# Performance work log

Hardware: AMD Instinct MI355X
Metric: run time of the kernel (lower is better)

## Reference

```python
import jax, jax.numpy as jnp
import numpy as np

EMB = 64
N_NODES = 50000
N_EDGES = 800000

def _mlp(h, W1, b1, W2, b2):
    h = jax.nn.relu(h @ W1 + b1)
    return jax.nn.relu(h @ W2 + b2)

def setup_inputs() -> dict:
    key = jax.random.key(0)
    ks = jax.random.split(key, 12)
    s = 1.0 / np.sqrt(3 * EMB)
    s2 = 1.0 / np.sqrt(EMB)
    x = jax.random.normal(ks[0], (N_NODES, 2 * EMB), dtype=jnp.float32)
    edge_index = jax.random.randint(ks[1], (2, N_EDGES), 0, N_NODES, dtype=jnp.int32)
    edge_attr = jax.random.normal(ks[2], (N_EDGES, EMB), dtype=jnp.float32)
    u = jax.random.normal(ks[3], (64, 64), dtype=jnp.float32)
    batch = jax.random.randint(ks[4], (N_NODES,), 0, 64, dtype=jnp.int32)
    W1a = jax.random.uniform(ks[5], (3 * EMB, EMB), jnp.float32, -s, s)
    b1a = jax.random.uniform(ks[6], (EMB,), jnp.float32, -s, s)
    W1b = jax.random.uniform(ks[7], (EMB, EMB), jnp.float32, -s2, s2)
    b1b = jax.random.uniform(ks[8], (EMB,), jnp.float32, -s2, s2)
    W2a = jax.random.uniform(ks[9], (3 * EMB, EMB), jnp.float32, -s, s)
    b2a = jax.random.uniform(ks[10], (EMB,), jnp.float32, -s, s)
    W2b = jax.random.uniform(ks[11], (EMB, EMB), jnp.float32, -s2, s2)
    b2b = jax.random.uniform(jax.random.fold_in(key, 99), (EMB,), jnp.float32, -s2, s2)
    return {"x": x, "edge_index": edge_index, "edge_attr": edge_attr, "u": u, "batch": batch,
            "W1a": W1a, "b1a": b1a, "W1b": W1b, "b1b": b1b,
            "W2a": W2a, "b2a": b2a, "W2b": W2b, "b2b": b2b}

def reference(x, edge_index, edge_attr, u, batch, W1a, b1a, W1b, b1b, W2a, b2a, W2b, b2b):
    senders, receivers = edge_index[0], edge_index[1]
    # gather sender node features [E, 2*EMB] and concat edge features -> [E, 3*EMB]
    msg = jnp.concatenate([x[senders], edge_attr], axis=1)
    msg = _mlp(msg, W1a, b1a, W1b, b1b)  # [E, EMB]
    agg = jax.ops.segment_sum(msg, receivers, num_segments=x.shape[0])  # [N, EMB]
    h = jnp.concatenate([x, agg], axis=1)  # [N, 3*EMB]
    return _mlp(h, W2a, b2a, W2b, b2b)  # [N, EMB]
```

## Files before the change

### kernel.cpp

```cpp
#include <hip/hip_runtime.h>
#include <hip/hip_bf16.h>

typedef __attribute__((ext_vector_type(8))) __bf16 bf16x8;
typedef __attribute__((ext_vector_type(4))) __bf16 bf16x4;
typedef __attribute__((ext_vector_type(2))) __bf16 bf16x2;
typedef __attribute__((ext_vector_type(4))) float f32x4;

#define MFMA(a, b, c) __builtin_amdgcn_mfma_f32_16x16x32_bf16((a), (b), (c), 0, 0, 0)

__device__ __forceinline__ bf16x8 pack8(f32x4 a, f32x4 b) {
    bf16x8 r;
    r[0] = (__bf16)a[0]; r[1] = (__bf16)a[1]; r[2] = (__bf16)a[2]; r[3] = (__bf16)a[3];
    r[4] = (__bf16)b[0]; r[5] = (__bf16)b[1]; r[6] = (__bf16)b[2]; r[7] = (__bf16)b[3];
    return r;
}

__device__ __forceinline__ bf16x8 cvt8(const float* __restrict__ p) {
    return pack8(*(const f32x4*)(p), *(const f32x4*)(p + 4));
}

__global__ __launch_bounds__(256) void zero_i32(int* __restrict__ p, int n) {
    for (int i = blockIdx.x * blockDim.x + threadIdx.x; i < n;
         i += gridDim.x * blockDim.x)
        p[i] = 0;
}

__global__ __launch_bounds__(256) void precompute_y(
    const float* __restrict__ x,
    const float* __restrict__ W1a, const float* __restrict__ b1a,
    const float* __restrict__ W2a, const float* __restrict__ b2a,
    float* __restrict__ y1, float* __restrict__ y2,
    int N, int ntiles)
{
    const int LDK = 136;
    __shared__ __align__(16) __bf16 w1t[64 * 136];
    __shared__ __align__(16) __bf16 w2t[64 * 136];
    for (int idx = threadIdx.x; idx < 64 * 128; idx += 256) {
        int k = idx >> 6, n = idx & 63;
        w1t[n * LDK + k] = (__bf16)W1a[k * 64 + n];
        w2t[n * LDK + k] = (__bf16)W2a[k * 64 + n];
    }
    __syncthreads();

    const int lane = threadIdx.x & 63, wave = threadIdx.x >> 6;
    const int l15 = lane & 15, l4 = lane >> 4;

    f32x4 bias1[4], bias2[4];
#pragma unroll
    for (int nt = 0; nt < 4; ++nt) {
        bias1[nt] = *(const f32x4*)(b1a + nt * 16 + l4 * 4);
        bias2[nt] = *(const f32x4*)(b2a + nt * 16 + l4 * 4);
    }

    for (int tile = blockIdx.x * 4 + wave; tile < ntiles; tile += gridDim.x * 4) {
        const int node = tile * 16 + l15;
        const int nrow = min(node, N - 1);
        f32x4 acc1[4], acc2[4];
#pragma unroll
        for (int nt = 0; nt < 4; ++nt) {
            acc1[nt] = (f32x4){0.f, 0.f, 0.f, 0.f};
            acc2[nt] = (f32x4){0.f, 0.f, 0.f, 0.f};
        }
#pragma unroll
        for (int j = 0; j < 4; ++j) {
            const int k0 = j * 32 + l4 * 8;
            bf16x8 b = cvt8(x + (size_t)nrow * 128 + k0);
#pragma unroll
            for (int nt = 0; nt < 4; ++nt) {
                bf16x8 a1 = *(const bf16x8*)(w1t + (nt * 16 + l15) * LDK + k0);
                acc1[nt] = MFMA(a1, b, acc1[nt]);
                bf16x8 a2 = *(const bf16x8*)(w2t + (nt * 16 + l15) * LDK + k0);
                acc2[nt] = MFMA(a2, b, acc2[nt]);
            }
        }
        if (node < N) {
#pragma unroll
            for (int nt = 0; nt < 4; ++nt) {
                f32x4 v1 = acc1[nt] + bias1[nt];
                f32x4 v2 = acc2[nt] + bias2[nt];
                *(f32x4*)(y1 + (size_t)node * 64 + nt * 16 + l4 * 4) = v1;
                *(f32x4*)(y2 + (size_t)node * 64 + nt * 16 + l4 * 4) = v2;
            }
        }
    }
}

__global__ __launch_bounds__(256) void hist_kernel(
    const int* __restrict__ recv, int* __restrict__ cnt, int E)
{
    for (int e = blockIdx.x * blockDim.x + threadIdx.x; e < E;
         e += gridDim.x * blockDim.x)
        atomicAdd(&cnt[recv[e]], 1);
}

__global__ __launch_bounds__(1024) void scan_offsets(
    const int* __restrict__ cnt, int* __restrict__ offs, int* __restrict__ cur, int N)
{
    __shared__ int wsum[16];
    __shared__ int stot;
    const int tid = threadIdx.x;
    const int lane = tid & 63, wave = tid >> 6;
    int carry = 0;
    const int CH = 4096;
    for (int base = 0; base < N; base += CH) {
        const int idx = base + tid * 4;
        int v0 = (idx + 0 < N) ? cnt[idx + 0] : 0;
        int v1 = (idx + 1 < N) ? cnt[idx + 1] : 0;
        int v2 = (idx + 2 < N) ? cnt[idx + 2] : 0;
        int v3 = (idx + 3 < N) ? cnt[idx + 3] : 0;
        const int t = v0 + v1 + v2 + v3;
        int s = t;
#pragma unroll
        for (int d = 1; d < 64; d <<= 1) {
            int u = __shfl_up(s, d);
            if (lane >= d) s += u;
        }
        if (lane == 63) wsum[wave] = s;
        __syncthreads();
        if (wave == 0) {
            int w = (lane < 16) ? wsum[lane] : 0;
            int ws = w;
#pragma unroll
            for (int d = 1; d < 16; d <<= 1) {
                int u = __shfl_up(ws, d);
                if (lane >= d) ws += u;
            }
            if (lane < 16) wsum[lane] = ws - w;
            if (lane == 15) stot = ws;
        }
        __syncthreads();
        const int excl = s - t + wsum[wave] + carry;
        if (idx + 0 < N) { offs[idx+0] = excl;                cur[idx+0] = excl; }
        if (idx + 1 < N) { offs[idx+1] = excl+v0;             cur[idx+1] = excl+v0; }
        if (idx + 2 < N) { offs[idx+2] = excl+v0+v1;          cur[idx+2] = excl+v0+v1; }
        if (idx + 3 < N) { offs[idx+3] = excl+v0+v1+v2;       cur[idx+3] = excl+v0+v1+v2; }
        carry += stot;
        __syncthreads();
    }
    if (tid == 0) offs[N] = carry;
}

template<int MODE>
__global__ __launch_bounds__(256) void edge_mlp(
    const float* __restrict__ eattr,
    const int* __restrict__ send, const int* __restrict__ recv,
    const float* __restrict__ W1a, const float* __restrict__ W1b,
    const float* __restrict__ b1b,
    const float* __restrict__ y1,
    int* __restrict__ cur, __bf16* __restrict__ msgC, float* agg,
    int E, int ntiles)
{
    const int LDK = 72;
    __shared__ __align__(16) __bf16 wat[64 * 72];
    __shared__ __align__(16) __bf16 wbt[64 * 72];
    __shared__ __align__(16) __bf16 hbuf[4][16 * 72];
    for (int idx = threadIdx.x; idx < 64 * 64; idx += 256) {
        int k = idx >> 6, n = idx & 63;
        wat[n * LDK + k] = (__bf16)W1a[(128 + k) * 64 + n];
        wbt[n * LDK + k] = (__bf16)W1b[k * 64 + n];
    }
    __syncthreads();

    const int lane = threadIdx.x & 63, wave = threadIdx.x >> 6;
    const int l15 = lane & 15, l4 = lane >> 4;
    __bf16* hb = hbuf[wave];

    f32x4 biasb[4];
#pragma unroll
    for (int nt = 0; nt < 4; ++nt) biasb[nt] = *(const f32x4*)(b1b + nt * 16 + l4 * 4);

    int tile = blockIdx.x * 4 + wave;
    const int stride = gridDim.x * 4;
    if (tile >= ntiles) return;

    int e  = tile * 16 + l15;
    int el = min(e, E - 1);
    int s  = send[el];
    int rv = recv[el];
    f32x4 ea[4], cin[4];
    {
        const float* ep = eattr + (size_t)el * 64 + l4 * 8;
        ea[0] = *(const f32x4*)(ep);      ea[1] = *(const f32x4*)(ep + 4);
        ea[2] = *(const f32x4*)(ep + 32); ea[3] = *(const f32x4*)(ep + 36);
#pragma unroll
        for (int nt = 0; nt < 4; ++nt)
            cin[nt] = *(const f32x4*)(y1 + (size_t)s * 64 + nt * 16 + l4 * 4);
    }

    while (true) {
        const int tnext = tile + stride;
        const bool have_next = tnext < ntiles;
        int e_n = e, el_n = el, s_n = s, rv_n = rv;
        if (have_next) {
            e_n  = tnext * 16 + l15;
            el_n = min(e_n, E - 1);
            s_n  = send[el_n];
            rv_n = recv[el_n];
        }
        int p = 0;
        if (MODE == 0 && l4 == 0 && e < E) p = atomicAdd(&cur[rv], 1);

        f32x4 acc[4] = {cin[0], cin[1], cin[2], cin[3]};
#pragma unroll
        for (int j = 0; j < 2; ++j) {
            bf16x8 b = pack8(ea[2 * j], ea[2 * j + 1]);
            const int k0 = j * 32 + l4 * 8;
#pragma unroll
            for (int nt = 0; nt < 4; ++nt) {
                bf16x8 a = *(const bf16x8*)(wat + (nt * 16 + l15) * LDK + k0);
                acc[nt] = MFMA(a, b, acc[nt]);
            }
        }
        f32x4 ea_n[4], cin_n[4];
        if (have_next) {
            const float* ep = eattr + (size_t)el_n * 64 + l4 * 8;
            ea_n[0] = *(const f32x4*)(ep);      ea_n[1] = *(const f32x4*)(ep + 4);
            ea_n[2] = *(const f32x4*)(ep + 32); ea_n[3] = *(const f32x4*)(ep + 36);
#pragma unroll
            for (int nt = 0; nt < 4; ++nt)
                cin_n[nt] = *(const f32x4*)(y1 + (size_t)s_n * 64 + nt * 16 + l4 * 4);
        }
#pragma unroll
        for (int nt = 0; nt < 4; ++nt) {
            bf16x4 hv;
#pragma unroll
            for (int r = 0; r < 4; ++r) hv[r] = (__bf16)fmaxf(acc[nt][r], 0.f);
            *(bf16x4*)(hb + l15 * LDK + nt * 16 + l4 * 4) = hv;
        }
        f32x4 acc2[4];
#pragma unroll
        for (int nt = 0; nt < 4; ++nt) acc2[nt] = biasb[nt];
#pragma unroll
        for (int j = 0; j < 2; ++j) {
            const int k0 = j * 32 + l4 * 8;
            bf16x8 b = *(const bf16x8*)(hb + l15 * LDK + k0);
#pragma unroll
            for (int nt = 0; nt < 4; ++nt) {
                bf16x8 a = *(const bf16x8*)(wbt + (nt * 16 + l15) * LDK + k0);
                acc2[nt] = MFMA(a, b, acc2[nt]);
            }
        }
        if (MODE == 0) {
            const int pb = __shfl(p, l15);
            if (e < E) {
                __bf16* row = msgC + (size_t)pb * 64;
#pragma unroll
                for (int nt = 0; nt < 4; ++nt) {
                    bf16x4 mv;
#pragma unroll
                    for (int r = 0; r < 4; ++r) mv[r] = (__bf16)fmaxf(acc2[nt][r], 0.f);
                    *(bf16x4*)(row + nt * 16 + l4 * 4) = mv;
                }
            }
        } else {
            if (e < E) {
                float* base = agg + (size_t)rv * 64 + l4 * 4;
#pragma unroll
                for (int nt = 0; nt < 4; ++nt)
#pragma unroll
                    for (int r = 0; r < 4; ++r)
                        unsafeAtomicAdd(base + nt * 16 + r, fmaxf(acc2[nt][r], 0.f));
            }
        }
        if (!have_next) break;
        tile = tnext; e = e_n; el = el_n; s = s_n; rv = rv_n;
#pragma unroll
        for (int i = 0; i < 4; ++i) { ea[i] = ea_n[i]; cin[i] = cin_n[i]; }
    }
}

__global__ __launch_bounds__(256) void csr_reduce(
    const unsigned* __restrict__ msg_u,
    const int* __restrict__ offs,
    __bf16* __restrict__ aggB, int N)
{
    const int wave = threadIdx.x >> 6, lane = threadIdx.x & 63;
    const int half = lane >> 5, c = lane & 31;
    for (int node = blockIdx.x * 4 + wave; node < N; node += gridDim.x * 4) {
        const int oL = offs[node], oR = offs[node + 1];
        float ax = 0.f, ay = 0.f;
        for (int p = oL + half; p < oR; p += 2) {
            const unsigned u = msg_u[(size_t)p * 32 + c];
            ax += __uint_as_float(u << 16);
            ay += __uint_as_float(u & 0xffff0000u);
        }
        ax += __shfl_xor(ax, 32);
        ay += __shfl_xor(ay, 32);
        if (half == 0) {
            bf16x2 v; v[0] = (__bf16)ax; v[1] = (__bf16)ay;
            *(bf16x2*)(aggB + (size_t)node * 64 + c * 2) = v;
        }
    }
}

template<int AGGF32>
__global__ __launch_bounds__(256) void node_pass(
    const void* __restrict__ aggp,
    const float* __restrict__ W2a, const float* __restrict__ W2b,
    const float* __restrict__ b2b,
    const float* __restrict__ y2, float* __restrict__ out,
    int N, int ntiles)
{
    const int LDK = 72;
    __shared__ __align__(16) __bf16 wat[64 * 72];
    __shared__ __align__(16) __bf16 wbt[64 * 72];
    __shared__ __align__(16) __bf16 hbuf[4][16 * 72];
    for (int idx = threadIdx.x; idx < 64 * 64; idx += 256) {
        int k = idx >> 6, n = idx & 63;
        wat[n * LDK + k] = (__bf16)W2a[(128 + k) * 64 + n];
        wbt[n * LDK + k] = (__bf16)W2b[k * 64 + n];
    }
    __syncthreads();

    const int lane = threadIdx.x & 63, wave = threadIdx.x >> 6;
    const int l15 = lane & 15, l4 = lane >> 4;
    __bf16* hb = hbuf[wave];

    f32x4 biasb[4];
#pragma unroll
    for (int nt = 0; nt < 4; ++nt) biasb[nt] = *(const f32x4*)(b2b + nt * 16 + l4 * 4);

    for (int tile = blockIdx.x * 4 + wave; tile < ntiles; tile += gridDim.x * 4) {
        const int node = tile * 16 + l15;
        const int nrow = min(node, N - 1);

        f32x4 acc[4];
#pragma unroll
        for (int nt = 0; nt < 4; ++nt)
            acc[nt] = *(const f32x4*)(y2 + (size_t)nrow * 64 + nt * 16 + l4 * 4);
#pragma unroll
        for (int j = 0; j < 2; ++j) {
            const int k0 = j * 32 + l4 * 8;
            bf16x8 b;
            if (AGGF32) b = cvt8((const float*)aggp + (size_t)nrow * 64 + k0);
            else        b = *(const bf16x8*)((const __bf16*)aggp + (size_t)nrow * 64 + k0);
#pragma unroll
            for (int nt = 0; nt < 4; ++nt) {
                bf16x8 a = *(const bf16x8*)(wat + (nt * 16 + l15) * LDK + k0);
                acc[nt] = MFMA(a, b, acc[nt]);
            }
        }
#pragma unroll
        for (int nt = 0; nt < 4; ++nt) {
            bf16x4 hv;
#pragma unroll
            for (int r = 0; r < 4; ++r) hv[r] = (__bf16)fmaxf(acc[nt][r], 0.f);
            *(bf16x4*)(hb + l15 * LDK + nt * 16 + l4 * 4) = hv;
        }

        f32x4 acc2[4];
#pragma unroll
        for (int nt = 0; nt < 4; ++nt) acc2[nt] = biasb[nt];
#pragma unroll
        for (int j = 0; j < 2; ++j) {
            const int k0 = j * 32 + l4 * 8;
            bf16x8 b = *(const bf16x8*)(hb + l15 * LDK + k0);
#pragma unroll
            for (int nt = 0; nt < 4; ++nt) {
                bf16x8 a = *(const bf16x8*)(wbt + (nt * 16 + l15) * LDK + k0);
                acc2[nt] = MFMA(a, b, acc2[nt]);
            }
        }
        if (node < N) {
#pragma unroll
            for (int nt = 0; nt < 4; ++nt) {
                f32x4 v;
#pragma unroll
                for (int r = 0; r < 4; ++r) v[r] = fmaxf(acc2[nt][r], 0.f);
                *(f32x4*)(out + (size_t)node * 64 + nt * 16 + l4 * 4) = v;
            }
        }
    }
}

extern "C" void kernel_launch(void* const* d_in, const int* in_sizes, int n_in,
                              void* d_out, int out_size, void* d_ws, size_t ws_size,
                              hipStream_t stream) {
    const float* x     = (const float*)d_in[0];
    const int*   eidx  = (const int*)d_in[1];
    const float* eattr = (const float*)d_in[2];
    const float* W1a = (const float*)d_in[5];
    const float* b1a = (const float*)d_in[6];
    const float* W1b = (const float*)d_in[7];
    const float* b1b = (const float*)d_in[8];
    const float* W2a = (const float*)d_in[9];
    const float* b2a = (const float*)d_in[10];
    const float* W2b = (const float*)d_in[11];
    const float* b2b = (const float*)d_in[12];
    float* out = (float*)d_out;

    const int N = in_sizes[0] / 128;
    const int E = in_sizes[1] / 2;
    const int* send = eidx;
    const int* recv = eidx + E;

    const size_t NG = (size_t)N * 64;
    const size_t need = 2 * NG * sizeof(float) + (size_t)E * 64 * sizeof(__bf16)
                      + (size_t)3 * (N + 1) * sizeof(int);
    const bool big = ws_size >= need;

    const int ntilesN = (N + 15) / 16;
    const int ntilesE = (E + 15) / 16;
    int blkN = (ntilesN + 3) / 4;
    if (blkN > 1024) blkN = 1024;
    int blkE = (ntilesE + 3) / 4;
    if (blkE > 1280) blkE = 1280;
    int blkS = (E + 255) / 256;
    if (blkS > 1024) blkS = 1024;
    int blkR = (N + 3) / 4;
    if (blkR > 2048) blkR = 2048;

    if (big) {
        float*  y1   = (float*)d_ws;
        float*  y2   = y1 + NG;
        __bf16* msgC = (__bf16*)(y2 + NG);
        int*    cnt  = (int*)(msgC + (size_t)E * 64);
        int*    offs = cnt + (N + 1);
        int*    cur  = offs + (N + 1);
        __bf16* aggB = (__bf16*)y1;

        zero_i32<<<(N + 256) / 256, 256, 0, stream>>>(cnt, N + 1);
        hist_kernel<<<blkS, 256, 0, stream>>>(recv, cnt, E);
        scan_offsets<<<1, 1024, 0, stream>>>(cnt, offs, cur, N);
        precompute_y<<<blkN, 256, 0, stream>>>(x, W1a, b1a, W2a, b2a, y1, y2, N, ntilesN);
        edge_mlp<0><<<blkE, 256, 0, stream>>>(eattr, send, recv, W1a, W1b, b1b,
                                              y1, cur, msgC, nullptr, E, ntilesE);
        csr_reduce<<<blkR, 256, 0, stream>>>((const unsigned*)msgC, offs, aggB, N);
        node_pass<0><<<blkN, 256, 0, stream>>>(aggB, W2a, W2b, b2b, y2, out, N, ntilesN);
    } else {
        float* agg = (float*)d_ws;
        float* y1  = agg + NG;
        float* y2  = y1 + NG;
        zero_i32<<<2048, 256, 0, stream>>>((int*)agg, (int)NG);
        precompute_y<<<blkN, 256, 0, stream>>>(x, W1a, b1a, W2a, b2a, y1, y2, N, ntilesN);
        edge_mlp<1><<<blkE, 256, 0, stream>>>(eattr, send, recv, W1a, W1b, b1b,
                                              y1, nullptr, nullptr, agg, E, ntilesE);
        node_pass<1><<<blkN, 256, 0, stream>>>(agg, W2a, W2b, b2b, y2, out, N, ntilesN);
    }
}
```

Baseline: 249.4 us.

## Compute CSR slot ranks in histogram pass, drop edge-kernel atomics and prefetch

The histogram kernel now records each edge's rank within its receiver bucket. The edge MLP then computes its output slot as offs[recv]+rank with no atomic counter, so the per-edge atomicAdd on a cursor array and the shuffle go away. Shared-memory weight and hidden buffers are re-laid out into 8-element fragment chunks with padding to cut bank conflicts. The manual software prefetch of the next tile is removed and the edge grid cap is raised. The cost is an extra E-sized rank array write and read, plus losing explicit load latency hiding.

Result: faster. 243.9 us (-2.2%).

```diff
diff --git a/kernel.cpp b/kernel.cpp
--- a/kernel.cpp
+++ b/kernel.cpp
@@ -85,16 +85,17 @@
     }
 }
 
-__global__ __launch_bounds__(256) void hist_kernel(
-    const int* __restrict__ recv, int* __restrict__ cnt, int E)
+__global__ __launch_bounds__(256) void hist_rank(
+    const int* __restrict__ recv, int* __restrict__ cnt,
+    int* __restrict__ rank, int E)
 {
     for (int e = blockIdx.x * blockDim.x + threadIdx.x; e < E;
          e += gridDim.x * blockDim.x)
-        atomicAdd(&cnt[recv[e]], 1);
+        rank[e] = atomicAdd(&cnt[recv[e]], 1);
 }
 
 __global__ __launch_bounds__(1024) void scan_offsets(
-    const int* __restrict__ cnt, int* __restrict__ offs, int* __restrict__ cur, int N)
+    const int* __restrict__ cnt, int* __restrict__ offs, int N)
 {
     __shared__ int wsum[16];
     __shared__ int stot;
@@ -130,10 +131,10 @@
         }
         __syncthreads();
         const int excl = s - t + wsum[wave] + carry;
-        if (idx + 0 < N) { offs[idx+0] = excl;                cur[idx+0] = excl; }
-        if (idx + 1 < N) { offs[idx+1] = excl+v0;             cur[idx+1] = excl+v0; }
-        if (idx + 2 < N) { offs[idx+2] = excl+v0+v1;          cur[idx+2] = excl+v0+v1; }
-        if (idx + 3 < N) { offs[idx+3] = excl+v0+v1+v2;       cur[idx+3] = excl+v0+v1+v2; }
+        if (idx + 0 < N) offs[idx + 0] = excl;
+        if (idx + 1 < N) offs[idx + 1] = excl + v0;
+        if (idx + 2 < N) offs[idx + 2] = excl + v0 + v1;
+        if (idx + 3 < N) offs[idx + 3] = excl + v0 + v1 + v2;
         carry += stot;
         __syncthreads();
     }
@@ -144,106 +145,83 @@
 __global__ __launch_bounds__(256) void edge_mlp(
     const float* __restrict__ eattr,
     const int* __restrict__ send, const int* __restrict__ recv,
+    const int* __restrict__ rank, const int* __restrict__ offs,
     const float* __restrict__ W1a, const float* __restrict__ W1b,
     const float* __restrict__ b1b,
     const float* __restrict__ y1,
-    int* __restrict__ cur, __bf16* __restrict__ msgC, float* agg,
+    __bf16* __restrict__ msgC, float* agg,
     int E, int ntiles)
 {
-    const int LDK = 72;
-    __shared__ __align__(16) __bf16 wat[64 * 72];
-    __shared__ __align__(16) __bf16 wbt[64 * 72];
-    __shared__ __align__(16) __bf16 hbuf[4][16 * 72];
+    __shared__ __align__(16) __bf16 wfA[8 * 65 * 8];
+    __shared__ __align__(16) __bf16 wfB[8 * 65 * 8];
+    __shared__ __align__(16) __bf16 hfrag[4][8 * 17 * 8];
     for (int idx = threadIdx.x; idx < 64 * 64; idx += 256) {
-        int k = idx >> 6, n = idx & 63;
-        wat[n * LDK + k] = (__bf16)W1a[(128 + k) * 64 + n];
-        wbt[n * LDK + k] = (__bf16)W1b[k * 64 + n];
+        const int k = idx >> 6, n = idx & 63;
+        const int c = k >> 3, i = k & 7;
+        wfA[(c * 65 + n) * 8 + i] = (__bf16)W1a[(128 + k) * 64 + n];
+        wfB[(c * 65 + n) * 8 + i] = (__bf16)W1b[k * 64 + n];
     }
     __syncthreads();
 
     const int lane = threadIdx.x & 63, wave = threadIdx.x >> 6;
     const int l15 = lane & 15, l4 = lane >> 4;
-    __bf16* hb = hbuf[wave];
+    __bf16* hf = hfrag[wave];
 
     f32x4 biasb[4];
 #pragma unroll
     for (int nt = 0; nt < 4; ++nt) biasb[nt] = *(const f32x4*)(b1b + nt * 16 + l4 * 4);
 
-    int tile = blockIdx.x * 4 + wave;
-    const int stride = gridDim.x * 4;
-    if (tile >= ntiles) return;
-
-    int e  = tile * 16 + l15;
-    int el = min(e, E - 1);
-    int s  = send[el];
-    int rv = recv[el];
-    f32x4 ea[4], cin[4];
-    {
-        const float* ep = eattr + (size_t)el * 64 + l4 * 8;
-        ea[0] = *(const f32x4*)(ep);      ea[1] = *(const f32x4*)(ep + 4);
-        ea[2] = *(const f32x4*)(ep + 32); ea[3] = *(const f32x4*)(ep + 36);
+    for (int tile = blockIdx.x * 4 + wave; tile < ntiles; tile += gridDim.x * 4) {
+        const int e = tile * 16 + l15;
+        const int el = min(e, E - 1);
+        const int s = send[el];
+        int p = 0, rv = 0;
+        if (MODE == 0) {
+            rv = recv[el];
+            p = offs[rv] + rank[el];
+        } else {
+            rv = recv[el];
+        }
+
+        f32x4 acc[4];
 #pragma unroll
         for (int nt = 0; nt < 4; ++nt)
-            cin[nt] = *(const f32x4*)(y1 + (size_t)s * 64 + nt * 16 + l4 * 4);
-    }
-
-    while (true) {
-        const int tnext = tile + stride;
-        const bool have_next = tnext < ntiles;
-        int e_n = e, el_n = el, s_n = s, rv_n = rv;
-        if (have_next) {
-            e_n  = tnext * 16 + l15;
-            el_n = min(e_n, E - 1);
-            s_n  = send[el_n];
-            rv_n = recv[el_n];
-        }
-        int p = 0;
-        if (MODE == 0 && l4 == 0 && e < E) p = atomicAdd(&cur[rv], 1);
-
-        f32x4 acc[4] = {cin[0], cin[1], cin[2], cin[3]};
+            acc[nt] = *(const f32x4*)(y1 + (size_t)s * 64 + nt * 16 + l4 * 4);
 #pragma unroll
         for (int j = 0; j < 2; ++j) {
-            bf16x8 b = pack8(ea[2 * j], ea[2 * j + 1]);
-            const int k0 = j * 32 + l4 * 8;
-#pragma unroll
-            for (int nt = 0; nt < 4; ++nt) {
-                bf16x8 a = *(const bf16x8*)(wat + (nt * 16 + l15) * LDK + k0);
+            const float* ep = eattr + (size_t)el * 64 + j * 32 + l4 * 8;
+            bf16x8 b = pack8(*(const f32x4*)ep, *(const f32x4*)(ep + 4));
+            const int c = j * 4 + l4;
+#pragma unroll
+            for (int nt = 0; nt < 4; ++nt) {
+                bf16x8 a = *(const bf16x8*)(wfA + ((c * 65) + nt * 16 + l15) * 8);
                 acc[nt] = MFMA(a, b, acc[nt]);
             }
-        }
-        f32x4 ea_n[4], cin_n[4];
-        if (have_next) {
-            const float* ep = eattr + (size_t)el_n * 64 + l4 * 8;
-            ea_n[0] = *(const f32x4*)(ep);      ea_n[1] = *(const f32x4*)(ep + 4);
-            ea_n[2] = *(const f32x4*)(ep + 32); ea_n[3] = *(const f32x4*)(ep + 36);
-#pragma unroll
-            for (int nt = 0; nt < 4; ++nt)
-                cin_n[nt] = *(const f32x4*)(y1 + (size_t)s_n * 64 + nt * 16 + l4 * 4);
         }
 #pragma unroll
         for (int nt = 0; nt < 4; ++nt) {
             bf16x4 hv;
 #pragma unroll
             for (int r = 0; r < 4; ++r) hv[r] = (__bf16)fmaxf(acc[nt][r], 0.f);
-            *(bf16x4*)(hb + l15 * LDK + nt * 16 + l4 * 4) = hv;
+            const int c2 = nt * 2 + (l4 >> 1);
+            *(bf16x4*)(hf + (c2 * 17 + l15) * 8 + (l4 & 1) * 4) = hv;
         }
         f32x4 acc2[4];
 #pragma unroll
         for (int nt = 0; nt < 4; ++nt) acc2[nt] = biasb[nt];
 #pragma unroll
         for (int j = 0; j < 2; ++j) {
-            const int k0 = j * 32 + l4 * 8;
-            bf16x8 b = *(const bf16x8*)(hb + l15 * LDK + k0);
-#pragma unroll
-            for (int nt = 0; nt < 4; ++nt) {
-                bf16x8 a = *(const bf16x8*)(wbt + (nt * 16 + l15) * LDK + k0);
+            const int c = j * 4 + l4;
+            bf16x8 b = *(const bf16x8*)(hf + (c * 17 + l15) * 8);
+#pragma unroll
+            for (int nt = 0; nt < 4; ++nt) {
+                bf16x8 a = *(const bf16x8*)(wfB + ((c * 65) + nt * 16 + l15) * 8);
                 acc2[nt] = MFMA(a, b, acc2[nt]);
             }
         }
-        if (MODE == 0) {
-            const int pb = __shfl(p, l15);
-            if (e < E) {
-                __bf16* row = msgC + (size_t)pb * 64;
+        if (e < E) {
+            if (MODE == 0) {
+                __bf16* row = msgC + (size_t)p * 64;
 #pragma unroll
                 for (int nt = 0; nt < 4; ++nt) {
                     bf16x4 mv;
@@ -251,9 +229,7 @@
                     for (int r = 0; r < 4; ++r) mv[r] = (__bf16)fmaxf(acc2[nt][r], 0.f);
                     *(bf16x4*)(row + nt * 16 + l4 * 4) = mv;
                 }
-            }
-        } else {
-            if (e < E) {
+            } else {
                 float* base = agg + (size_t)rv * 64 + l4 * 4;
 #pragma unroll
                 for (int nt = 0; nt < 4; ++nt)
@@ -262,10 +238,6 @@
                         unsafeAtomicAdd(base + nt * 16 + r, fmaxf(acc2[nt][r], 0.f));
             }
         }
-        if (!have_next) break;
-        tile = tnext; e = e_n; el = el_n; s = s_n; rv = rv_n;
-#pragma unroll
-        for (int i = 0; i < 4; ++i) { ea[i] = ea_n[i]; cin[i] = cin_n[i]; }
     }
 }
 
@@ -396,7 +368,7 @@
 
     const size_t NG = (size_t)N * 64;
     const size_t need = 2 * NG * sizeof(float) + (size_t)E * 64 * sizeof(__bf16)
-                      + (size_t)3 * (N + 1) * sizeof(int);
+                      + ((size_t)2 * (N + 1) + E) * sizeof(int);
     const bool big = ws_size >= need;
 
     const int ntilesN = (N + 15) / 16;
@@ -404,7 +376,7 @@
     int blkN = (ntilesN + 3) / 4;
     if (blkN > 1024) blkN = 1024;
     int blkE = (ntilesE + 3) / 4;
-    if (blkE > 1280) blkE = 1280;
+    if (blkE > 1536) blkE = 1536;
     int blkS = (E + 255) / 256;
     if (blkS > 1024) blkS = 1024;
     int blkR = (N + 3) / 4;
@@ -416,15 +388,15 @@
         __bf16* msgC = (__bf16*)(y2 + NG);
         int*    cnt  = (int*)(msgC + (size_t)E * 64);
         int*    offs = cnt + (N + 1);
-        int*    cur  = offs + (N + 1);
+        int*    rank = offs + (N + 1);
         __bf16* aggB = (__bf16*)y1;
 
         zero_i32<<<(N + 256) / 256, 256, 0, stream>>>(cnt, N + 1);
-        hist_kernel<<<blkS, 256, 0, stream>>>(recv, cnt, E);
-        scan_offsets<<<1, 1024, 0, stream>>>(cnt, offs, cur, N);
+        hist_rank<<<blkS, 256, 0, stream>>>(recv, cnt, rank, E);
+        scan_offsets<<<1, 1024, 0, stream>>>(cnt, offs, N);
         precompute_y<<<blkN, 256, 0, stream>>>(x, W1a, b1a, W2a, b2a, y1, y2, N, ntilesN);
-        edge_mlp<0><<<blkE, 256, 0, stream>>>(eattr, send, recv, W1a, W1b, b1b,
-                                              y1, cur, msgC, nullptr, E, ntilesE);
+        edge_mlp<0><<<blkE, 256, 0, stream>>>(eattr, send, recv, rank, offs,
+                                              W1a, W1b, b1b, y1, msgC, nullptr, E, ntilesE);
         csr_reduce<<<blkR, 256, 0, stream>>>((const unsigned*)msgC, offs, aggB, N);
         node_pass<0><<<blkN, 256, 0, stream>>>(aggB, W2a, W2b, b2b, y2, out, N, ntilesN);
     } else {
@@ -433,8 +405,8 @@
         float* y2  = y1 + NG;
         zero_i32<<<2048, 256, 0, stream>>>((int*)agg, (int)NG);
         precompute_y<<<blkN, 256, 0, stream>>>(x, W1a, b1a, W2a, b2a, y1, y2, N, ntilesN);
-        edge_mlp<1><<<blkE, 256, 0, stream>>>(eattr, send, recv, W1a, W1b, b1b,
-                                              y1, nullptr, nullptr, agg, E, ntilesE);
+        edge_mlp<1><<<blkE, 256, 0, stream>>>(eattr, send, recv, nullptr, nullptr,
+                                              W1a, W1b, b1b, y1, nullptr, agg, E, ntilesE);
         node_pass<1><<<blkN, 256, 0, stream>>>(agg, W2a, W2b, b2b, y2, out, N, ntilesN);
     }
 }
```
